# Optimization experiments

Measured on AMD Instinct MI355X. Metric: run time of the kernel, lower is better.

## Reference

```python
import jax, jax.numpy as jnp
import numpy as np

B, D, H = 4096, 66, 512  # batch, system dim (22 atoms * 3), MLP hidden


def _dynamics(t, xs, W1, b1, W2, b2, W3, b3):
    # CNF vector field f(t, x): 3-layer SiLU MLP on concat([x, t])
    h = jnp.concatenate([xs, t], axis=1)          # [B, D+1]
    h = jax.nn.silu(h @ W1 + b1)                  # [B, H]
    h = jax.nn.silu(h @ W2 + b2)                  # [B, H]
    return h @ W3 + b3                            # [B, D]


def setup_inputs() -> dict:
    key = jax.random.key(0)
    ks = jax.random.split(key, 5)
    xs = jax.random.normal(ks[0], (B, D), dtype=jnp.float32)
    t = jax.random.uniform(ks[1], (B, 1), dtype=jnp.float32)
    W1 = jax.random.normal(ks[2], (D + 1, H), dtype=jnp.float32) / np.float32(np.sqrt(D + 1))
    b1 = jnp.zeros((H,), dtype=jnp.float32)
    W2 = jax.random.normal(ks[3], (H, H), dtype=jnp.float32) / np.float32(np.sqrt(H))
    b2 = jnp.zeros((H,), dtype=jnp.float32)
    W3 = jax.random.normal(ks[4], (H, D), dtype=jnp.float32) / np.float32(np.sqrt(H))
    b3 = jnp.zeros((D,), dtype=jnp.float32)
    return {"xs": xs, "t": t, "W1": W1, "b1": b1, "W2": W2, "b2": b2, "W3": W3, "b3": b3}


def reference(xs, t, W1, b1, W2, b2, W3, b3):
    # Exact divergence: trace of Jacobian d f / d x, computed with D JVPs
    # (forward-mode equivalent of the torch per-dim autograd.grad loop).
    def f(x):
        return _dynamics(t, x, W1, b1, W2, b2, W3, b3)

    dxs = f(xs)                                   # [B, D]
    eye = jnp.eye(D, dtype=xs.dtype)              # basis vectors e_i

    def jvp_col(e):
        _, tang = jax.jvp(f, (xs,), (jnp.broadcast_to(e, xs.shape),))
        return tang                               # J @ e_i, shape [B, D]

    tangs = jax.vmap(jvp_col)(eye)                # [D, B, D]
    div = jnp.einsum('dbd->b', tangs)             # sum_i (J e_i)_i = tr(J)
    return dxs, -div[:, None]
```

## Files before the change

kernel.cpp:

```cpp
#include <hip/hip_runtime.h>

#define Bn 4096
#define Dn 66
#define Hn 512

typedef __attribute__((ext_vector_type(8))) short short8;
typedef __attribute__((ext_vector_type(4))) float f32x4;

__device__ __forceinline__ unsigned short f2bf(float x) {
    union { float f; unsigned u; } v; v.f = x;
    unsigned r = v.u + 0x7fffu + ((v.u >> 16) & 1u);
    return (unsigned short)(r >> 16);
}
__device__ __forceinline__ float bf2f(unsigned short h) {
    union { float f; unsigned u; } v; v.u = ((unsigned)h) << 16; return v.f;
}


__global__ __launch_bounds__(512, 2) void k_h1pack(
    const float* __restrict__ xs, const float* __restrict__ tt,
    const float* __restrict__ W1, const float* __restrict__ b1,
    const float* __restrict__ W2, const float* __restrict__ W3,
    unsigned short* __restrict__ WQ, unsigned short* __restrict__ W3P,
    unsigned short* __restrict__ h1hiP, unsigned short* __restrict__ s1P)
{
    __shared__ float sLds[16*68];
    const int bid = blockIdx.x, tid = threadIdx.x;
    const int lane = tid & 63, wv = tid >> 6;

    if (bid < 512) {
        const int rt = bid >> 1, half = bid & 1;
        const int r0 = rt*16;
        for (int idx = tid; idx < 67*16; idx += 512) {
            const int i = idx >> 4, r = idx & 15;
            sLds[idx] = (i < Dn) ? xs[(size_t)(r0+r)*Dn + i] : tt[r0+r];
        }
        __syncthreads();
        const int rg = lane & 7, cg = lane >> 3;
        const int ks = half*8 + wv;
        const int c0 = ks*32 + cg*4;
        const int irot = (bid >> 3) & 31;
        float z[2][4];
        {
            const float4 b4 = *(const float4*)&b1[c0];
            z[0][0]=b4.x; z[0][1]=b4.y; z[0][2]=b4.z; z[0][3]=b4.w;
            z[1][0]=b4.x; z[1][1]=b4.y; z[1][2]=b4.z; z[1][3]=b4.w;
        }
        #pragma unroll 2
        for (int s = 0; s < 67; ++s) {
            int i = s + irot; if (i >= 67) i -= 67;
            const float2 xf = *(const float2*)&sLds[i*16 + 2*rg];
            const float4 wA = *(const float4*)&W1[(size_t)i*Hn + c0];
            const float ww[4] = {wA.x, wA.y, wA.z, wA.w};
            #pragma unroll
            for (int j = 0; j < 4; ++j) {
                z[0][j] = fmaf(xf.x, ww[j], z[0][j]);
                z[1][j] = fmaf(xf.y, ww[j], z[1][j]);
            }
        }
        const int kgrp = cg >> 1, joff = (cg & 1)*4;
        #pragma unroll
        for (int rr = 0; rr < 2; ++rr) {
            const int r = 2*rg + rr;
            ushort4 phi, ps;
            unsigned short* PH = (unsigned short*)&phi;
            unsigned short* PS = (unsigned short*)&ps;
            #pragma unroll
            for (int j = 0; j < 4; ++j) {
                const float zv = z[rr][j];
                const float sg = 1.f / (1.f + __expf(-zv));
                PH[j] = f2bf(zv * sg);
                PS[j] = f2bf(sg * (1.f + zv * (1.f - sg)));
            }
            const size_t off = ((size_t)(rt*16 + ks)*64 + r + 16*kgrp)*8 + joff;
            *(ushort4*)&h1hiP[off] = phi;
            *(ushort4*)&s1P [off] = ps;
        }
    } else if (bid < 576) {
        const int pb = bid - 512;
        const int ct = pb >> 1;
        {
            const int r = tid >> 5, ii = tid & 31;
            const float* src = &W3[(size_t)(ct*16 + r)*Dn];
            sLds[r*68 + ii] = src[ii];
            sLds[r*68 + ii + 32] = src[ii + 32];
            if (ii < 2) sLds[r*68 + ii + 64] = src[ii + 64];
        }
        __syncthreads();
        const int ks = (pb & 1)*8 + wv;
        const int n = lane & 15, kg = lane >> 4;
        const int c = ct*16 + n;
        const int abase = ks*32 + kg*8;
        float w2v[8], m[8];
        #pragma unroll
        for (int j = 0; j < 8; ++j) {
            w2v[j] = W2[(size_t)(abase + j)*Hn + c];
            m[j] = 0.f;
        }
        #pragma unroll 2
        for (int i = 0; i < Dn; ++i) {
            const float w3 = sLds[n*68 + i];
            const float4 w1a = *(const float4*)&W1[(size_t)i*Hn + abase];
            const float4 w1b = *(const float4*)&W1[(size_t)i*Hn + abase + 4];
            m[0] = fmaf(w3, w1a.x, m[0]); m[1] = fmaf(w3, w1a.y, m[1]);
            m[2] = fmaf(w3, w1a.z, m[2]); m[3] = fmaf(w3, w1a.w, m[3]);
            m[4] = fmaf(w3, w1b.x, m[4]); m[5] = fmaf(w3, w1b.y, m[5]);
            m[6] = fmaf(w3, w1b.z, m[6]); m[7] = fmaf(w3, w1b.w, m[7]);
        }
        short8 pw, pc;
        #pragma unroll
        for (int j = 0; j < 8; ++j) {
            pw[j] = (short)f2bf(w2v[j]);
            pc[j] = (short)f2bf(w2v[j] * m[j]);
        }
        const size_t off = ((size_t)(ct*16 + ks)*64 + lane)*16;
        *(short8*)&WQ[off]     = pw;
        *(short8*)&WQ[off + 8] = pc;
    } else {
        const int tix = (bid - 576)*8 + wv;
        if (tix < 80) {
            const int ks = tix & 15;
            const int n = lane & 15, kg = lane >> 4;
            const int j_out = (tix >> 4)*16 + n;
            const int abase = ks*32 + kg*8;
            short8 p;
            #pragma unroll
            for (int j = 0; j < 8; ++j)
                p[j] = (j_out < Dn) ? (short)f2bf(W3[(size_t)(abase + j)*Dn + j_out]) : (short)0;
            *(short8*)&W3P[((size_t)tix*64 + lane)*8] = p;
        }
    }
}

__global__ __launch_bounds__(1024, 4) void k_BC(
    const unsigned short* __restrict__ h1hiP, const unsigned short* __restrict__ s1P,
    const unsigned short* __restrict__ WQ, const float* __restrict__ b2,
    const unsigned short* __restrict__ W3P, const float* __restrict__ b3,
    float* __restrict__ out)
{
    __shared__ __align__(16) unsigned short sH[8192];
    __shared__ __align__(16) unsigned short sL[8192];
    __shared__ float sRed[16*16];

    const int tid = threadIdx.x, lane = tid & 63, wv = tid >> 6;
    const int rt = blockIdx.x, r0 = rt*16;
    const int n = lane & 15, kg = lane >> 4;
    const int rot = (blockIdx.x >> 3) & 15;

    const int ctb = wv*2;
    f32x4 zac[2], vac[2];
    #pragma unroll
    for (int ti = 0; ti < 2; ++ti) {
        const float bz = b2[(ctb + ti)*16 + n];
        zac[ti] = (f32x4){bz, bz, bz, bz};
        vac[ti] = (f32x4){0.f, 0.f, 0.f, 0.f};
    }
    short8 wbuf[2][2], qbuf[2][2], abuf[2], sbuf[2];
    {
        const size_t ao = ((size_t)(rt*16 + rot)*64 + lane)*8;
        abuf[0] = *(const short8*)&h1hiP[ao];
        sbuf[0] = *(const short8*)&s1P[ao];
        #pragma unroll
        for (int ti = 0; ti < 2; ++ti) {
            const size_t wo = ((size_t)((ctb + ti)*16 + rot)*64 + lane)*16;
            wbuf[0][ti] = *(const short8*)&WQ[wo];
            qbuf[0][ti] = *(const short8*)&WQ[wo + 8];
        }
    }
    #pragma unroll
    for (int s = 0; s < 16; ++s) {
        const int cur = s & 1, nxt = cur ^ 1;
        if (s < 15) {
            const int ksn = (s + 1 + rot) & 15;
            const size_t ao = ((size_t)(rt*16 + ksn)*64 + lane)*8;
            abuf[nxt] = *(const short8*)&h1hiP[ao];
            sbuf[nxt] = *(const short8*)&s1P[ao];
            #pragma unroll
            for (int ti = 0; ti < 2; ++ti) {
                const size_t wo = ((size_t)((ctb + ti)*16 + ksn)*64 + lane)*16;
                wbuf[nxt][ti] = *(const short8*)&WQ[wo];
                qbuf[nxt][ti] = *(const short8*)&WQ[wo + 8];
            }
        }
        #pragma unroll
        for (int ti = 0; ti < 2; ++ti) {
            zac[ti] = __builtin_amdgcn_mfma_f32_16x16x32_bf16(abuf[cur], wbuf[cur][ti], zac[ti], 0, 0, 0);
            vac[ti] = __builtin_amdgcn_mfma_f32_16x16x32_bf16(sbuf[cur], qbuf[cur][ti], vac[ti], 0, 0, 0);
        }
    }

    float dp[4] = {0.f, 0.f, 0.f, 0.f};
    #pragma unroll
    for (int ti = 0; ti < 2; ++ti) {
        const int c = (ctb + ti)*16 + n;
        const int ks2 = c >> 5, kg2 = (c >> 3) & 3, j2 = c & 7;
        #pragma unroll
        for (int q = 0; q < 4; ++q) {
            const float z2 = zac[ti][q];
            const float sg = 1.f / (1.f + __expf(-z2));
            const float h2 = z2 * sg;
            dp[q] = fmaf(sg * (1.f + z2 * (1.f - sg)), vac[ti][q], dp[q]);
            const unsigned short hh = f2bf(h2);
            const int o = (ks2*64 + (kg*4 + q) + 16*kg2)*8 + j2;
            sH[o] = hh;
            sL[o] = f2bf(h2 - bf2f(hh));
        }
    }
    #pragma unroll
    for (int q = 0; q < 4; ++q) {
        float v = dp[q];
        v += __shfl_xor(v, 1, 64);
        v += __shfl_xor(v, 2, 64);
        v += __shfl_xor(v, 4, 64);
        v += __shfl_xor(v, 8, 64);
        if (n == 0) sRed[wv*16 + kg*4 + q] = v;
    }
    __syncthreads();

    if (tid < 16) {
        float s = 0.f;
        #pragma unroll
        for (int q = 0; q < 16; ++q) s += sRed[q*16 + tid];
        out[(size_t)Bn*Dn + r0 + tid] = -s;
    }

    if (wv < 5) {
        const int jt = wv;
        const int j = jt*16 + n;
        const float bj = (j < Dn) ? b3[j] : 0.f;
        f32x4 oac = (f32x4){bj, bj, bj, bj};
        #pragma unroll 4
        for (int s = 0; s < 16; ++s) {
            const int ks = (s + rot) & 15;
            const int aoff = (ks*64 + lane)*8;
            const short8 ahi = *(const short8*)&sH[aoff];
            const short8 alo = *(const short8*)&sL[aoff];
            const short8 wf  = *(const short8*)&W3P[((size_t)(jt*16 + ks)*64 + lane)*8];
            oac = __builtin_amdgcn_mfma_f32_16x16x32_bf16(ahi, wf, oac, 0, 0, 0);
            oac = __builtin_amdgcn_mfma_f32_16x16x32_bf16(alo, wf, oac, 0, 0, 0);
        }
        if (j < Dn) {
            #pragma unroll
            for (int q = 0; q < 4; ++q)
                out[(size_t)(r0 + kg*4 + q)*Dn + j] = oac[q];
        }
    }
}

extern "C" void kernel_launch(void* const* d_in, const int* in_sizes, int n_in,
                              void* d_out, int out_size, void* d_ws, size_t ws_size,
                              hipStream_t stream)
{
    const float* xs = (const float*)d_in[0];
    const float* t  = (const float*)d_in[1];
    const float* W1 = (const float*)d_in[2];
    const float* b1 = (const float*)d_in[3];
    const float* W2 = (const float*)d_in[4];
    const float* b2 = (const float*)d_in[5];
    const float* W3 = (const float*)d_in[6];
    const float* b3 = (const float*)d_in[7];
    float* out = (float*)d_out;

    char* ws = (char*)d_ws;
    unsigned short* WQ   = (unsigned short*)(ws);
    unsigned short* W3P  = (unsigned short*)(ws + 1048576);
    unsigned short* h1hi = (unsigned short*)(ws + 1130496);
    unsigned short* s1   = (unsigned short*)(ws + 5324800);

    k_h1pack<<<586, 512,  0, stream>>>(xs, t, W1, b1, W2, W3, WQ, W3P, h1hi, s1);
    k_BC    <<<256, 1024, 0, stream>>>(h1hi, s1, WQ, b2, W3P, b3, out);
}
```

Baseline: 106.1 us.

## Fuse layer-1 computation into main kernel, keep h1 and SiLU' in LDS

Moves the first-layer matmul and SiLU/derivative computation from the pack kernel into the main per-row-tile kernel, storing the bf16 activations and slopes in shared memory instead of round-tripping them through global workspace. The pack kernel now only prepares weight buffers, with far fewer blocks. This removes the global writes and reads of the h1 and s1 intermediates. In exchange the main kernel uses more LDS, which may lower occupancy, and each block now runs a serial first-layer phase before its MFMA loop, with only 256 blocks to hide that latency.

```diff
diff --git a/kernel.cpp b/kernel.cpp
--- a/kernel.cpp
+++ b/kernel.cpp
@@ -17,67 +17,17 @@
 }
 
 
-__global__ __launch_bounds__(512, 2) void k_h1pack(
-    const float* __restrict__ xs, const float* __restrict__ tt,
-    const float* __restrict__ W1, const float* __restrict__ b1,
-    const float* __restrict__ W2, const float* __restrict__ W3,
-    unsigned short* __restrict__ WQ, unsigned short* __restrict__ W3P,
-    unsigned short* __restrict__ h1hiP, unsigned short* __restrict__ s1P)
+__global__ __launch_bounds__(512, 2) void k_pack(
+    const float* __restrict__ W1, const float* __restrict__ W2,
+    const float* __restrict__ W3,
+    unsigned short* __restrict__ WQ, unsigned short* __restrict__ W3P)
 {
     __shared__ float sLds[16*68];
     const int bid = blockIdx.x, tid = threadIdx.x;
     const int lane = tid & 63, wv = tid >> 6;
 
-    if (bid < 512) {
-        const int rt = bid >> 1, half = bid & 1;
-        const int r0 = rt*16;
-        for (int idx = tid; idx < 67*16; idx += 512) {
-            const int i = idx >> 4, r = idx & 15;
-            sLds[idx] = (i < Dn) ? xs[(size_t)(r0+r)*Dn + i] : tt[r0+r];
-        }
-        __syncthreads();
-        const int rg = lane & 7, cg = lane >> 3;
-        const int ks = half*8 + wv;
-        const int c0 = ks*32 + cg*4;
-        const int irot = (bid >> 3) & 31;
-        float z[2][4];
-        {
-            const float4 b4 = *(const float4*)&b1[c0];
-            z[0][0]=b4.x; z[0][1]=b4.y; z[0][2]=b4.z; z[0][3]=b4.w;
-            z[1][0]=b4.x; z[1][1]=b4.y; z[1][2]=b4.z; z[1][3]=b4.w;
-        }
-        #pragma unroll 2
-        for (int s = 0; s < 67; ++s) {
-            int i = s + irot; if (i >= 67) i -= 67;
-            const float2 xf = *(const float2*)&sLds[i*16 + 2*rg];
-            const float4 wA = *(const float4*)&W1[(size_t)i*Hn + c0];
-            const float ww[4] = {wA.x, wA.y, wA.z, wA.w};
-            #pragma unroll
-            for (int j = 0; j < 4; ++j) {
-                z[0][j] = fmaf(xf.x, ww[j], z[0][j]);
-                z[1][j] = fmaf(xf.y, ww[j], z[1][j]);
-            }
-        }
-        const int kgrp = cg >> 1, joff = (cg & 1)*4;
-        #pragma unroll
-        for (int rr = 0; rr < 2; ++rr) {
-            const int r = 2*rg + rr;
-            ushort4 phi, ps;
-            unsigned short* PH = (unsigned short*)&phi;
-            unsigned short* PS = (unsigned short*)&ps;
-            #pragma unroll
-            for (int j = 0; j < 4; ++j) {
-                const float zv = z[rr][j];
-                const float sg = 1.f / (1.f + __expf(-zv));
-                PH[j] = f2bf(zv * sg);
-                PS[j] = f2bf(sg * (1.f + zv * (1.f - sg)));
-            }
-            const size_t off = ((size_t)(rt*16 + ks)*64 + r + 16*kgrp)*8 + joff;
-            *(ushort4*)&h1hiP[off] = phi;
-            *(ushort4*)&s1P [off] = ps;
-        }
-    } else if (bid < 576) {
-        const int pb = bid - 512;
+    if (bid < 64) {
+        const int pb = bid;
         const int ct = pb >> 1;
         {
             const int r = tid >> 5, ii = tid & 31;
@@ -117,12 +67,12 @@
         *(short8*)&WQ[off]     = pw;
         *(short8*)&WQ[off + 8] = pc;
     } else {
-        const int tix = (bid - 576)*8 + wv;
+        const int tix = (bid - 64)*8 + wv;
         if (tix < 80) {
             const int ks = tix & 15;
-            const int n = lane & 15, kg = lane >> 4;
+            const int n = lane & 15;
             const int j_out = (tix >> 4)*16 + n;
-            const int abase = ks*32 + kg*8;
+            const int abase = ks*32 + (lane >> 4)*8;
             short8 p;
             #pragma unroll
             for (int j = 0; j < 8; ++j)
@@ -132,12 +82,16 @@
     }
 }
 
-__global__ __launch_bounds__(1024, 4) void k_BC(
-    const unsigned short* __restrict__ h1hiP, const unsigned short* __restrict__ s1P,
+__global__ __launch_bounds__(1024, 4) void k_fused(
+    const float* __restrict__ xs, const float* __restrict__ tt,
+    const float* __restrict__ W1, const float* __restrict__ b1,
     const unsigned short* __restrict__ WQ, const float* __restrict__ b2,
     const unsigned short* __restrict__ W3P, const float* __restrict__ b3,
     float* __restrict__ out)
 {
+    __shared__ float sX[67*16];
+    __shared__ __align__(16) unsigned short sA[8192];
+    __shared__ __align__(16) unsigned short sS[8192];
     __shared__ __align__(16) unsigned short sH[8192];
     __shared__ __align__(16) unsigned short sL[8192];
     __shared__ float sRed[16*16];
@@ -145,7 +99,57 @@
     const int tid = threadIdx.x, lane = tid & 63, wv = tid >> 6;
     const int rt = blockIdx.x, r0 = rt*16;
     const int n = lane & 15, kg = lane >> 4;
-    const int rot = (blockIdx.x >> 3) & 15;
+    const int rot = (rt >> 3) & 15;
+
+    for (int idx = tid; idx < 67*16; idx += 1024) {
+        const int i = idx >> 4, r = idx & 15;
+        sX[idx] = (i < Dn) ? xs[(size_t)(r0+r)*Dn + i] : tt[r0+r];
+    }
+    __syncthreads();
+
+    {
+        const int rg = lane & 7, cg = lane >> 3;
+        const int ks = wv;
+        const int c0 = ks*32 + cg*4;
+        const int irot = (rt >> 3) & 31;
+        float z[2][4];
+        {
+            const float4 b4 = *(const float4*)&b1[c0];
+            z[0][0]=b4.x; z[0][1]=b4.y; z[0][2]=b4.z; z[0][3]=b4.w;
+            z[1][0]=b4.x; z[1][1]=b4.y; z[1][2]=b4.z; z[1][3]=b4.w;
+        }
+        #pragma unroll 2
+        for (int s = 0; s < 67; ++s) {
+            int i = s + irot; if (i >= 67) i -= 67;
+            const float2 xf = *(const float2*)&sX[i*16 + 2*rg];
+            const float4 wA = *(const float4*)&W1[(size_t)i*Hn + c0];
+            const float ww[4] = {wA.x, wA.y, wA.z, wA.w};
+            #pragma unroll
+            for (int j = 0; j < 4; ++j) {
+                z[0][j] = fmaf(xf.x, ww[j], z[0][j]);
+                z[1][j] = fmaf(xf.y, ww[j], z[1][j]);
+            }
+        }
+        const int kgrp = cg >> 1, joff = (cg & 1)*4;
+        #pragma unroll
+        for (int rr = 0; rr < 2; ++rr) {
+            const int r = 2*rg + rr;
+            ushort4 phi, ps;
+            unsigned short* PH = (unsigned short*)&phi;
+            unsigned short* PS = (unsigned short*)&ps;
+            #pragma unroll
+            for (int j = 0; j < 4; ++j) {
+                const float zv = z[rr][j];
+                const float sg = 1.f / (1.f + __expf(-zv));
+                PH[j] = f2bf(zv * sg);
+                PS[j] = f2bf(sg * (1.f + zv * (1.f - sg)));
+            }
+            const int off = ((ks)*64 + r + 16*kgrp)*8 + joff;
+            *(ushort4*)&sA[off] = phi;
+            *(ushort4*)&sS[off] = ps;
+        }
+    }
+    __syncthreads();
 
     const int ctb = wv*2;
     f32x4 zac[2], vac[2];
@@ -157,12 +161,12 @@
     }
     short8 wbuf[2][2], qbuf[2][2], abuf[2], sbuf[2];
     {
-        const size_t ao = ((size_t)(rt*16 + rot)*64 + lane)*8;
-        abuf[0] = *(const short8*)&h1hiP[ao];
-        sbuf[0] = *(const short8*)&s1P[ao];
+        const int ks0 = rot;
+        abuf[0] = *(const short8*)&sA[(ks0*64 + lane)*8];
+        sbuf[0] = *(const short8*)&sS[(ks0*64 + lane)*8];
         #pragma unroll
         for (int ti = 0; ti < 2; ++ti) {
-            const size_t wo = ((size_t)((ctb + ti)*16 + rot)*64 + lane)*16;
+            const size_t wo = ((size_t)((ctb + ti)*16 + ks0)*64 + lane)*16;
             wbuf[0][ti] = *(const short8*)&WQ[wo];
             qbuf[0][ti] = *(const short8*)&WQ[wo + 8];
         }
@@ -172,9 +176,8 @@
         const int cur = s & 1, nxt = cur ^ 1;
         if (s < 15) {
             const int ksn = (s + 1 + rot) & 15;
-            const size_t ao = ((size_t)(rt*16 + ksn)*64 + lane)*8;
-            abuf[nxt] = *(const short8*)&h1hiP[ao];
-            sbuf[nxt] = *(const short8*)&s1P[ao];
+            abuf[nxt] = *(const short8*)&sA[(ksn*64 + lane)*8];
+            sbuf[nxt] = *(const short8*)&sS[(ksn*64 + lane)*8];
             #pragma unroll
             for (int ti = 0; ti < 2; ++ti) {
                 const size_t wo = ((size_t)((ctb + ti)*16 + ksn)*64 + lane)*16;
@@ -262,11 +265,9 @@
     float* out = (float*)d_out;
 
     char* ws = (char*)d_ws;
-    unsigned short* WQ   = (unsigned short*)(ws);
-    unsigned short* W3P  = (unsigned short*)(ws + 1048576);
-    unsigned short* h1hi = (unsigned short*)(ws + 1130496);
-    unsigned short* s1   = (unsigned short*)(ws + 5324800);
-
-    k_h1pack<<<586, 512,  0, stream>>>(xs, t, W1, b1, W2, W3, WQ, W3P, h1hi, s1);
-    k_BC    <<<256, 1024, 0, stream>>>(h1hi, s1, WQ, b2, W3P, b3, out);
-}
+    unsigned short* WQ  = (unsigned short*)(ws);
+    unsigned short* W3P = (unsigned short*)(ws + 1048576);
+
+    k_pack <<<74,  512,  0, stream>>>(W1, W2, W3, WQ, W3P);
+    k_fused<<<256, 1024, 0, stream>>>(xs, t, W1, b1, WQ, b2, W3P, b3, out);
+}
```

Result: no change. 106.7 us (+0.6%).
